# Kernel tuning notes

Hardware: AMD Instinct MI355X
Metric: run time of the kernel (lower is better)

## Reference

```python
import jax, jax.numpy as jnp
import numpy as np

N = 20000      # nodes
E = 160000     # edges
F_IN = 128     # node_feature_dim
HID = 128      # hidden_dim
HEADS = 8
G = 64         # graphs in batch


def setup_inputs() -> dict:
    key = jax.random.key(0)
    ks = iter(jax.random.split(key, 40))

    def w(shape, fan):
        return jax.random.normal(next(ks), shape, jnp.float32) / np.sqrt(fan)

    inp = {}
    inp['x'] = jax.random.normal(next(ks), (N, F_IN), jnp.float32)
    inp['edge_index'] = jax.random.randint(next(ks), (2, E), 0, N, jnp.int32)
    inp['batch'] = jnp.sort(jax.random.randint(next(ks), (N,), 0, G, jnp.int32))
    # initial projection
    inp['Wp'] = w((F_IN, HID), F_IN); inp['bp'] = jnp.zeros((HID,), jnp.float32)
    # layers 0..2: TransformerConv(HID -> HID//HEADS per head, heads=HEADS, concat) => heads*out = HID
    inp['Wq'] = w((3, HID, HID), HID); inp['bq'] = jnp.zeros((3, HID), jnp.float32)
    inp['Wk'] = w((3, HID, HID), HID); inp['bk'] = jnp.zeros((3, HID), jnp.float32)
    inp['Wv'] = w((3, HID, HID), HID); inp['bv'] = jnp.zeros((3, HID), jnp.float32)
    inp['Ws'] = w((3, HID, HID), HID); inp['bs'] = jnp.zeros((3, HID), jnp.float32)
    inp['Wbeta'] = w((3, 3 * HID, 1), 3 * HID)
    # layer 3: TransformerConv(HID -> HID per head, heads=HEADS, concat=False -> head mean)
    inp['Wq3'] = w((HID, HEADS * HID), HID); inp['bq3'] = jnp.zeros((HEADS * HID,), jnp.float32)
    inp['Wk3'] = w((HID, HEADS * HID), HID); inp['bk3'] = jnp.zeros((HEADS * HID,), jnp.float32)
    inp['Wv3'] = w((HID, HEADS * HID), HID); inp['bv3'] = jnp.zeros((HEADS * HID,), jnp.float32)
    inp['Ws3'] = w((HID, HID), HID); inp['bs3'] = jnp.zeros((HID,), jnp.float32)
    inp['Wbeta3'] = w((3 * HID, 1), 3 * HID)
    # batchnorm affine params for 4 layers
    inp['bn_gamma'] = jnp.ones((4, HID), jnp.float32)
    inp['bn_beta'] = jnp.zeros((4, HID), jnp.float32)
    return inp


def _tconv(x, src, dst, Wq, bq, Wk, bk, Wv, bv, Ws, bs, Wb, heads, concat):
    n = x.shape[0]
    d = Wq.shape[1] // heads  # per-head dim
    q = (x @ Wq + bq).reshape(n, heads, d)
    k = (x @ Wk + bk).reshape(n, heads, d)
    v = (x @ Wv + bv).reshape(n, heads, d)
    # per-edge attention logits [E, heads]
    logits = jnp.einsum('ehd,ehd->eh', q[dst], k[src]) / jnp.sqrt(jnp.float32(d))
    # segment softmax over incoming edges of each target node
    m = jax.ops.segment_max(logits, dst, num_segments=n)
    m = jnp.where(jnp.isfinite(m), m, 0.0)
    ex = jnp.exp(logits - m[dst])
    denom = jax.ops.segment_sum(ex, dst, num_segments=n)
    a = ex / (denom[dst] + 1e-16)  # [E, heads]
    out = jax.ops.segment_sum(a[:, :, None] * v[src], dst, num_segments=n)  # [n, heads, d]
    out = out.reshape(n, heads * d) if concat else out.mean(axis=1)
    # beta-gated skip connection
    r = x @ Ws + bs
    g = jax.nn.sigmoid(jnp.concatenate([out, r, out - r], axis=-1) @ Wb)  # [n, 1]
    return g * r + (1.0 - g) * out


def _bn(x, gamma, beta):
    mu = x.mean(axis=0)
    var = x.var(axis=0)
    return (x - mu) * jax.lax.rsqrt(var + 1e-5) * gamma + beta


def reference(x, edge_index, batch, Wp, bp, Wq, bq, Wk, bk, Wv, bv, Ws, bs, Wbeta,
              Wq3, bq3, Wk3, bk3, Wv3, bv3, Ws3, bs3, Wbeta3, bn_gamma, bn_beta):
    src, dst = edge_index[0], edge_index[1]
    h = x @ Wp + bp
    for i in range(3):
        h = _tconv(h, src, dst, Wq[i], bq[i], Wk[i], bk[i], Wv[i], bv[i],
                   Ws[i], bs[i], Wbeta[i], HEADS, concat=True)
        h = jax.nn.relu(_bn(h, bn_gamma[i], bn_beta[i]))
    h = _tconv(h, src, dst, Wq3, bq3, Wk3, bk3, Wv3, bv3, Ws3, bs3, Wbeta3,
               HEADS, concat=False)
    h = jax.nn.relu(_bn(h, bn_gamma[3], bn_beta[3]))
    # global mean pool per graph
    sums = jax.ops.segment_sum(h, batch, num_segments=G)
    cnt = jax.ops.segment_sum(jnp.ones((h.shape[0],), h.dtype), batch, num_segments=G)
    return sums / jnp.maximum(cnt, 1.0)[:, None]
```

## Files before the change

### kernel.cpp

```cpp
#include <hip/hip_runtime.h>
#include <math.h>

#define NNODES 20000
#define NPAD   20096
#define NEDGES 160000
#define HIDDIM 128
#define NHEADS 8
#define NGRAPH 64
#define KC 384
#define GXTILES 157

typedef short short8 __attribute__((ext_vector_type(8)));
typedef float floatx4 __attribute__((ext_vector_type(4)));
typedef unsigned short ushort4v __attribute__((ext_vector_type(4)));

__device__ inline unsigned short f2bf(float x) {
    unsigned u = __float_as_uint(x);
    u += 0x7fff + ((u >> 16) & 1);
    return (unsigned short)(u >> 16);
}
__device__ inline float bf2f(unsigned short h) {
    return __uint_as_float(((unsigned)h) << 16);
}

__device__ __forceinline__ void gload16(const unsigned short* g, unsigned short* l) {
    __builtin_amdgcn_global_load_lds(
        (const __attribute__((address_space(1))) unsigned int*)g,
        (__attribute__((address_space(3))) unsigned int*)l, 16, 0, 0);
}

__global__ __launch_bounds__(256) void zero_kernel(float* __restrict__ p, int n) {
    int i = blockIdx.x * blockDim.x + threadIdx.x;
    if (i < n) p[i] = 0.f;
}

__global__ __launch_bounds__(256) void count_deg_kernel(const int* __restrict__ dst,
                                                        int* __restrict__ deg, int e) {
    int i = blockIdx.x * blockDim.x + threadIdx.x;
    if (i < e) atomicAdd(&deg[dst[i]], 1);
}

__global__ __launch_bounds__(256) void scan1_kernel(const int* __restrict__ deg,
                                                    int* __restrict__ chunk,
                                                    int* __restrict__ bsum, int n) {
    __shared__ int buf[256];
    int t = threadIdx.x;
    int i = blockIdx.x * 256 + t;
    int v = (i < n) ? deg[i] : 0;
    buf[t] = v;
    __syncthreads();
    for (int off = 1; off < 256; off <<= 1) {
        int tmp = (t >= off) ? buf[t - off] : 0;
        __syncthreads();
        buf[t] += tmp;
        __syncthreads();
    }
    if (i < n) chunk[i] = buf[t];
    if (t == 255) bsum[blockIdx.x] = buf[255];
}

__global__ __launch_bounds__(128) void scan2_kernel(int* __restrict__ bsum, int nb) {
    __shared__ int buf[128];
    int t = threadIdx.x;
    int v = (t < nb) ? bsum[t] : 0;
    buf[t] = v;
    __syncthreads();
    for (int off = 1; off < 128; off <<= 1) {
        int tmp = (t >= off) ? buf[t - off] : 0;
        __syncthreads();
        buf[t] += tmp;
        __syncthreads();
    }
    if (t < nb) bsum[t] = buf[t] - v;
}

__global__ __launch_bounds__(256) void scan3_kernel(const int* __restrict__ chunk,
                                                    const int* __restrict__ bsum,
                                                    int* __restrict__ offs, int n) {
    int i = blockIdx.x * 256 + threadIdx.x;
    if (i < n) offs[i + 1] = chunk[i] + bsum[i >> 8];
    if (i == 0) offs[0] = 0;
}

__global__ __launch_bounds__(256) void scatter_gb_kernel(
    const int* __restrict__ src, const int* __restrict__ dst,
    const int* __restrict__ offs, int* __restrict__ cursor,
    int* __restrict__ csr_src, int e,
    const int* __restrict__ batch, int* __restrict__ gs, int* __restrict__ ge, int n) {
    int i = blockIdx.x * blockDim.x + threadIdx.x;
    if (i < e) {
        int d = dst[i];
        int pos = offs[d] + atomicAdd(&cursor[d], 1);
        csr_src[pos] = src[i];
    }
    if (i < n) {
        int b = batch[i];
        if (i == 0 || batch[i - 1] != b) gs[b] = i;
        if (i == n - 1 || batch[i + 1] != b) ge[b] = i + 1;
    }
}

__global__ __launch_bounds__(128) void prep_all_kernel(
    const float* __restrict__ Wq, const float* __restrict__ Wk,
    const float* __restrict__ Wv, const float* __restrict__ Ws,
    const float* __restrict__ Wp, const float* __restrict__ Ws3,
    const float* __restrict__ bq, const float* __restrict__ bk,
    const float* __restrict__ bv, const float* __restrict__ bs,
    const float* __restrict__ bs3,
    const float* __restrict__ Wq3, const float* __restrict__ Wk3,
    const float* __restrict__ bq3,
    const float* __restrict__ Wv3, const float* __restrict__ bv3,
    unsigned short* __restrict__ WtAll, float* __restrict__ bcat,
    unsigned short* __restrict__ Wvm, float* __restrict__ bvm) {
    int id = blockIdx.x;
    int k = threadIdx.x;
    if (id >= 3861) {
        int j = id - 3861;
#pragma unroll
        for (int h = 0; h < 8; ++h) {
            float w = Wv3[(size_t)k * 1024 + h * 128 + j] * 0.125f;
            Wvm[(size_t)j * 1024 + h * 128 + k] = f2bf(w);
        }
        if (k == 0) {
            float s = 0.f;
            for (int h = 0; h < 8; ++h) s += bv3[h * 128 + j];
            bvm[j] = s * 0.125f;
        }
        return;
    }
    if (id >= 2837) {
        int hb = id - 2837;
        int h = hb >> 7, b = hb & 127;
        __shared__ float wk[128];
        wk[k] = Wk3[(size_t)b * 1024 + h * 128 + k];
        __syncthreads();
        const float* wq = Wq3 + (size_t)k * 1024 + h * 128;
        float acc = 0.f;
#pragma unroll 16
        for (int d = 0; d < 128; ++d) acc = fmaf(wq[d], wk[d], acc);
        unsigned short hi = f2bf(acc);
        unsigned short lo = f2bf(acc - bf2f(hi));
        unsigned short* dst = WtAll + (size_t)(1664 + h * 128 + b) * KC;
        dst[k] = hi;
        dst[128 + k] = hi;
        dst[256 + k] = lo;
        if (k == 0) {
            float bb = 0.f;
            for (int d = 0; d < 128; ++d) bb = fmaf(bq3[h * 128 + d], wk[d], bb);
            bcat[1536 + h * 128 + b] = bb;
        }
        return;
    }
    if (id >= 2816) {
        int idx = (id - 2816) * 128 + k;
        if (idx >= 2688) return;
        float v;
        if (idx < 1536) {
            int li = idx / 512, n = idx % 512, sel = n >> 7, np = n & 127;
            const float* b = (sel == 0) ? bq : (sel == 1) ? bk : (sel == 2) ? bv : bs;
            v = b[li * 128 + np];
        } else if (idx < 2560) {
            return;
        } else {
            v = bs3[idx - 2560];
        }
        bcat[idx] = v;
        return;
    }
    float w;
    if (id < 1536) {
        int li = id / 512, n = id % 512, sel = n >> 7, np = n & 127;
        const float* W = (sel == 0) ? Wq : (sel == 1) ? Wk : (sel == 2) ? Wv : Ws;
        w = W[li * 16384 + k * 128 + np];
    } else if (id < 1664) {
        w = Wp[k * 128 + (id - 1536)];
    } else if (id < 2688) {
        return;
    } else {
        w = Ws3[k * 128 + (id - 2688)];
    }
    unsigned short hi = f2bf(w);
    unsigned short lo = f2bf(w - bf2f(hi));
    unsigned short* dst = WtAll + (size_t)id * KC;
    dst[k] = hi;
    dst[128 + k] = hi;
    dst[256 + k] = lo;
}

__global__ __launch_bounds__(256) void cat_from_kernel(const float* __restrict__ h,
                                                       unsigned short* __restrict__ Acat) {
    int idx = blockIdx.x * 256 + threadIdx.x;
    if (idx >= NPAD * HIDDIM) return;
    int r = idx >> 7, k = idx & 127;
    float x = (r < NNODES) ? h[idx] : 0.f;
    unsigned short hi = f2bf(x);
    unsigned short lo = f2bf(x - bf2f(hi));
    unsigned short* row = Acat + (size_t)r * KC;
    row[k] = hi;
    row[128 + k] = lo;
    row[256 + k] = hi;
}

template <typename OutT, int KG, int BY, int ST, int OMODE>
__global__ __launch_bounds__(256) void gemm_lds_kernel(
    const unsigned short* __restrict__ A, const unsigned short* __restrict__ Wt,
    const float* __restrict__ bias, OutT* __restrict__ C, int M, int nrows) {
    int id = blockIdx.x;
    int xcd = id & 7;
    int idx = id >> 3;
    int bx = (idx / BY) * 8 + xcd;
    int by = idx % BY;
    if (bx >= GXTILES) return;

    __shared__ unsigned short lds[2][2][4096];

    int tid = threadIdx.x;
    int lane = tid & 63;
    int wave = tid >> 6;
    int m = lane & 15;
    int q = lane >> 4;
    int nodeBase = bx * 128 + (wave & 1) * 64;
    int featBase = by * 128 + (wave >> 1) * 64;

    const unsigned short* gA = A + (size_t)bx * 128 * ST;
    const unsigned short* gW = Wt + (size_t)by * 128 * ST;

    int rs = lane >> 2;
    int cp0 = lane & 3;

    auto stagef = [&](int buf, int kk) {
        int kof = kk * 32;
#pragma unroll
        for (int jj = 0; jj < 2; ++jj) {
            int j = wave * 2 + jj;
            int row = j * 16 + rs;
            int g = cp0 ^ ((row >> 1) & 3);
            gload16(gA + (size_t)row * ST + kof + g * 8,
                    &lds[buf][0][0] + (size_t)j * 512);
            gload16(gW + (size_t)row * ST + kof + g * 8,
                    &lds[buf][1][0] + (size_t)j * 512);
        }
    };

    floatx4 acc[4][4];
#pragma unroll
    for (int r = 0; r < 4; ++r)
#pragma unroll
        for (int c = 0; c < 4; ++c) acc[r][c] = (floatx4){0.f, 0.f, 0.f, 0.f};

    stagef(0, 0);
    __syncthreads();

    for (int kg = 0; kg < KG; ++kg) {
        int cur = kg & 1;
        if (kg + 1 < KG) stagef(cur ^ 1, kg + 1);
        short8 a[4], b[4];
#pragma unroll
        for (int r = 0; r < 4; ++r) {
            int wr = (wave >> 1) * 64 + r * 16 + m;
            int cp = q ^ ((wr >> 1) & 3);
            a[r] = *(const short8*)(&lds[cur][1][0] + wr * 32 + cp * 8);
        }
#pragma unroll
        for (int c = 0; c < 4; ++c) {
            int ar = (wave & 1) * 64 + c * 16 + m;
            int cp = q ^ ((ar >> 1) & 3);
            b[c] = *(const short8*)(&lds[cur][0][0] + ar * 32 + cp * 8);
        }
#pragma unroll
        for (int r = 0; r < 4; ++r)
#pragma unroll
            for (int c = 0; c < 4; ++c)
                acc[r][c] = __builtin_amdgcn_mfma_f32_16x16x32_bf16(a[r], b[c], acc[r][c], 0, 0, 0);
        __syncthreads();
    }

    float4 bv[4];
#pragma unroll
    for (int r = 0; r < 4; ++r) bv[r] = *(const float4*)(bias + featBase + r * 16 + q * 4);
#pragma unroll
    for (int c = 0; c < 4; ++c) {
        int node = nodeBase + c * 16 + m;
        if (node < nrows) {
#pragma unroll
            for (int r = 0; r < 4; ++r) {
                int f0 = featBase + r * 16 + q * 4;
                float v0 = acc[r][c][0] + bv[r].x;
                float v1 = acc[r][c][1] + bv[r].y;
                float v2 = acc[r][c][2] + bv[r].z;
                float v3 = acc[r][c][3] + bv[r].w;
                if (OMODE == 2) {
                    unsigned short* row = (unsigned short*)C + (size_t)node * KC;
                    unsigned short h0 = f2bf(v0), h1 = f2bf(v1), h2 = f2bf(v2), h3 = f2bf(v3);
                    ushort4v hiv = {h0, h1, h2, h3};
                    ushort4v lov = {f2bf(v0 - bf2f(h0)), f2bf(v1 - bf2f(h1)),
                                    f2bf(v2 - bf2f(h2)), f2bf(v3 - bf2f(h3))};
                    *(ushort4v*)(row + f0) = hiv;
                    *(ushort4v*)(row + 128 + f0) = lov;
                    *(ushort4v*)(row + 256 + f0) = hiv;
                } else if (OMODE == 1) {
                    ushort4v o = {f2bf(v0), f2bf(v1), f2bf(v2), f2bf(v3)};
                    *(ushort4v*)((unsigned short*)C + (size_t)node * M + f0) = o;
                } else {
                    float4 o = {v0, v1, v2, v3};
                    *(float4*)((float*)C + (size_t)node * M + f0) = o;
                }
            }
        }
    }
}

__global__ __launch_bounds__(64) void attn_small_kernel(
    const unsigned short* __restrict__ qkvs,
    const float* __restrict__ Wb,
    const int* __restrict__ offs, const int* __restrict__ csr_src,
    float* __restrict__ out) {
    int i = blockIdx.x;
    int l = threadIdx.x;
    int g = l >> 5;
    int d0 = (l & 31) * 4;
    uint2 qraw = *(const uint2*)(qkvs + (size_t)i * 512 + d0);
    uint2 rraw = *(const uint2*)(qkvs + (size_t)i * 512 + 384 + d0);
    float q0 = bf2f((unsigned short)(qraw.x & 0xffff)), q1 = bf2f((unsigned short)(qraw.x >> 16));
    float q2 = bf2f((unsigned short)(qraw.y & 0xffff)), q3 = bf2f((unsigned short)(qraw.y >> 16));
    int e0 = offs[i], e1 = offs[i + 1];
    float lac = 0.f;
    float a0 = 0.f, a1 = 0.f, a2 = 0.f, a3 = 0.f;
    int e = e0 + g;
    uint2 kk_n = {0, 0}, vv_n = {0, 0};
    if (e < e1) {
        int sn = csr_src[e];
        const unsigned short* row = qkvs + (size_t)sn * 512;
        kk_n = *(const uint2*)(row + 128 + d0);
        vv_n = *(const uint2*)(row + 256 + d0);
    }
    while (e < e1) {
        uint2 kk = kk_n, vv = vv_n;
        int en = e + 2;
        if (en < e1) {
            int sn2 = csr_src[en];
            const unsigned short* row2 = qkvs + (size_t)sn2 * 512;
            kk_n = *(const uint2*)(row2 + 128 + d0);
            vv_n = *(const uint2*)(row2 + 256 + d0);
        }
        float k0 = bf2f((unsigned short)(kk.x & 0xffff)), k1 = bf2f((unsigned short)(kk.x >> 16));
        float k2 = bf2f((unsigned short)(kk.y & 0xffff)), k3 = bf2f((unsigned short)(kk.y >> 16));
        float p = q0 * k0 + q1 * k1 + q2 * k2 + q3 * k3;
        p += __shfl_xor(p, 1);
        p += __shfl_xor(p, 2);
        float w = __expf(p * 0.25f);
        float v0 = bf2f((unsigned short)(vv.x & 0xffff)), v1 = bf2f((unsigned short)(vv.x >> 16));
        float v2 = bf2f((unsigned short)(vv.y & 0xffff)), v3 = bf2f((unsigned short)(vv.y >> 16));
        a0 += w * v0;
        a1 += w * v1;
        a2 += w * v2;
        a3 += w * v3;
        lac += w;
        e = en;
    }
    a0 += __shfl_xor(a0, 32);
    a1 += __shfl_xor(a1, 32);
    a2 += __shfl_xor(a2, 32);
    a3 += __shfl_xor(a3, 32);
    lac += __shfl_xor(lac, 32);
    float inv = 1.f / (lac + 1e-16f);
    float o0 = a0 * inv, o1 = a1 * inv, o2 = a2 * inv, o3 = a3 * inv;
    float r0 = bf2f((unsigned short)(rraw.x & 0xffff)), r1 = bf2f((unsigned short)(rraw.x >> 16));
    float r2 = bf2f((unsigned short)(rraw.y & 0xffff)), r3 = bf2f((unsigned short)(rraw.y >> 16));
    float part = o0 * Wb[d0] + o1 * Wb[d0 + 1] + o2 * Wb[d0 + 2] + o3 * Wb[d0 + 3]
               + r0 * Wb[128 + d0] + r1 * Wb[128 + d0 + 1]
               + r2 * Wb[128 + d0 + 2] + r3 * Wb[128 + d0 + 3]
               + (o0 - r0) * Wb[256 + d0] + (o1 - r1) * Wb[256 + d0 + 1]
               + (o2 - r2) * Wb[256 + d0 + 2] + (o3 - r3) * Wb[256 + d0 + 3];
    if (g) part = 0.f;
#pragma unroll
    for (int msk = 1; msk <= 32; msk <<= 1) part += __shfl_xor(part, msk);
    float gg = 1.f / (1.f + __expf(-part));
    if (g == 0) {
        float4 o4 = {gg * r0 + (1.f - gg) * o0, gg * r1 + (1.f - gg) * o1,
                     gg * r2 + (1.f - gg) * o2, gg * r3 + (1.f - gg) * o3};
        *(float4*)(out + (size_t)i * HIDDIM + d0) = o4;
    }
}

__global__ __launch_bounds__(64) void attn_big_kernel(
    const unsigned short* __restrict__ tbuf, const unsigned short* __restrict__ Acat,
    const int* __restrict__ offs, const int* __restrict__ csr_src,
    unsigned short* __restrict__ agg) {
    int i = blockIdx.x;
    int l = threadIdx.x;
    int doff = (l & 7) * 16;
    const unsigned short* tp = tbuf + (size_t)i * 1152 + l * 16;
    uint4 t0 = *(const uint4*)tp;
    uint4 t1 = *(const uint4*)(tp + 8);
    float tq[16];
    tq[0] = bf2f((unsigned short)(t0.x & 0xffff)); tq[1] = bf2f((unsigned short)(t0.x >> 16));
    tq[2] = bf2f((unsigned short)(t0.y & 0xffff)); tq[3] = bf2f((unsigned short)(t0.y >> 16));
    tq[4] = bf2f((unsigned short)(t0.z & 0xffff)); tq[5] = bf2f((unsigned short)(t0.z >> 16));
    tq[6] = bf2f((unsigned short)(t0.w & 0xffff)); tq[7] = bf2f((unsigned short)(t0.w >> 16));
    tq[8] = bf2f((unsigned short)(t1.x & 0xffff)); tq[9] = bf2f((unsigned short)(t1.x >> 16));
    tq[10] = bf2f((unsigned short)(t1.y & 0xffff)); tq[11] = bf2f((unsigned short)(t1.y >> 16));
    tq[12] = bf2f((unsigned short)(t1.z & 0xffff)); tq[13] = bf2f((unsigned short)(t1.z >> 16));
    tq[14] = bf2f((unsigned short)(t1.w & 0xffff)); tq[15] = bf2f((unsigned short)(t1.w >> 16));
    int e0 = offs[i], e1 = offs[i + 1];
    float ac[16];
#pragma unroll
    for (int j = 0; j < 16; ++j) ac[j] = 0.f;
    float lac = 0.f;
    int e = e0;
    uint4 k0n = {0, 0, 0, 0}, k1n = {0, 0, 0, 0};
    if (e < e1) {
        const unsigned short* hp = Acat + (size_t)csr_src[e] * KC + doff;
        k0n = *(const uint4*)hp;
        k1n = *(const uint4*)(hp + 8);
    }
    while (e < e1) {
        uint4 k0 = k0n, k1 = k1n;
        int en = e + 1;
        if (en < e1) {
            const unsigned short* hp2 = Acat + (size_t)csr_src[en] * KC + doff;
            k0n = *(const uint4*)hp2;
            k1n = *(const uint4*)(hp2 + 8);
        }
        float kk[16];
        kk[0] = bf2f((unsigned short)(k0.x & 0xffff)); kk[1] = bf2f((unsigned short)(k0.x >> 16));
        kk[2] = bf2f((unsigned short)(k0.y & 0xffff)); kk[3] = bf2f((unsigned short)(k0.y >> 16));
        kk[4] = bf2f((unsigned short)(k0.z & 0xffff)); kk[5] = bf2f((unsigned short)(k0.z >> 16));
        kk[6] = bf2f((unsigned short)(k0.w & 0xffff)); kk[7] = bf2f((unsigned short)(k0.w >> 16));
        kk[8] = bf2f((unsigned short)(k1.x & 0xffff)); kk[9] = bf2f((unsigned short)(k1.x >> 16));
        kk[10] = bf2f((unsigned short)(k1.y & 0xffff)); kk[11] = bf2f((unsigned short)(k1.y >> 16));
        kk[12] = bf2f((unsigned short)(k1.z & 0xffff)); kk[13] = bf2f((unsigned short)(k1.z >> 16));
        kk[14] = bf2f((unsigned short)(k1.w & 0xffff)); kk[15] = bf2f((unsigned short)(k1.w >> 16));
        float p = 0.f;
#pragma unroll
        for (int j = 0; j < 16; ++j) p = fmaf(tq[j], kk[j], p);
        p += __shfl_xor(p, 1);
        p += __shfl_xor(p, 2);
        p += __shfl_xor(p, 4);
        float w = __expf(p * 0.08838834764831845f);
#pragma unroll
        for (int j = 0; j < 16; ++j) ac[j] = fmaf(w, kk[j], ac[j]);
        lac += w;
        e = en;
    }
    float inv = 1.f / (lac + 1e-16f);
    unsigned short* o = agg + (size_t)i * 1024 + l * 16;
    ushort4v o0 = {f2bf(ac[0] * inv), f2bf(ac[1] * inv), f2bf(ac[2] * inv), f2bf(ac[3] * inv)};
    ushort4v o1 = {f2bf(ac[4] * inv), f2bf(ac[5] * inv), f2bf(ac[6] * inv), f2bf(ac[7] * inv)};
    ushort4v o2 = {f2bf(ac[8] * inv), f2bf(ac[9] * inv), f2bf(ac[10] * inv), f2bf(ac[11] * inv)};
    ushort4v o3 = {f2bf(ac[12] * inv), f2bf(ac[13] * inv), f2bf(ac[14] * inv), f2bf(ac[15] * inv)};
    *(ushort4v*)o = o0;
    *(ushort4v*)(o + 4) = o1;
    *(ushort4v*)(o + 8) = o2;
    *(ushort4v*)(o + 12) = o3;
}

__global__ __launch_bounds__(128) void beta3_stats_kernel(
    const float* __restrict__ omean, const unsigned short* __restrict__ tbuf,
    const float* __restrict__ Wb, float* __restrict__ out,
    float* __restrict__ stat, int n, float* __restrict__ pool_out) {
    int t = threadIdx.x;
    if (blockIdx.x < NGRAPH) pool_out[blockIdx.x * HIDDIM + t] = 0.f;
    __shared__ float wsum[2];
    float s = 0.f, sq = 0.f;
    for (int i = blockIdx.x; i < n; i += gridDim.x) {
        float o = omean[(size_t)i * HIDDIM + t];
        float r = bf2f(tbuf[(size_t)i * 1152 + 1024 + t]);
        float part = o * Wb[t] + r * Wb[128 + t] + (o - r) * Wb[256 + t];
#pragma unroll
        for (int msk = 1; msk <= 32; msk <<= 1) part += __shfl_xor(part, msk);
        if ((t & 63) == 0) wsum[t >> 6] = part;
        __syncthreads();
        float tot = wsum[0] + wsum[1];
        __syncthreads();
        float g = 1.f / (1.f + __expf(-tot));
        float v = g * r + (1.f - g) * o;
        out[(size_t)i * HIDDIM + t] = v;
        s += v;
        sq += v * v;
    }
    atomicAdd(&stat[t], s);
    atomicAdd(&stat[HIDDIM + t], sq);
}

__global__ __launch_bounds__(128) void bn_stats_kernel(const float* __restrict__ x,
                                                       float* __restrict__ stat, int n) {
    int t = threadIdx.x;
    float s = 0.f, sq = 0.f;
    for (int i = blockIdx.x; i < n; i += gridDim.x) {
        float v = x[(size_t)i * HIDDIM + t];
        s += v;
        sq += v * v;
    }
    atomicAdd(&stat[t], s);
    atomicAdd(&stat[HIDDIM + t], sq);
}

__global__ __launch_bounds__(128) void bn_apply_kernel(float* __restrict__ x,
                                                       const float* __restrict__ stat,
                                                       const float* __restrict__ gamma,
                                                       const float* __restrict__ beta, int n,
                                                       unsigned short* __restrict__ cat) {
    int t = threadIdx.x;
    float mu = stat[t] / (float)n;
    float var = stat[HIDDIM + t] / (float)n - mu * mu;
    float rs = rsqrtf(var + 1e-5f);
    float g = gamma[t], b = beta[t];
    for (int i = blockIdx.x; i < n; i += gridDim.x) {
        float v = x[(size_t)i * HIDDIM + t];
        v = fmaxf((v - mu) * rs * g + b, 0.f);
        x[(size_t)i * HIDDIM + t] = v;
        if (cat) {
            unsigned short hi = f2bf(v);
            unsigned short lo = f2bf(v - bf2f(hi));
            unsigned short* row = cat + (size_t)i * KC;
            row[t] = hi;
            row[128 + t] = lo;
            row[256 + t] = hi;
        }
    }
}

__global__ __launch_bounds__(256) void pool_bn_part_kernel(
    const float* __restrict__ x, const float* __restrict__ stat,
    const float* __restrict__ gamma, const float* __restrict__ beta,
    const int* __restrict__ gs, const int* __restrict__ ge,
    float* __restrict__ out, int n) {
    int g = blockIdx.x, c = blockIdx.y;
    int t = threadIdx.x;
    int f = t & 127, half = t >> 7;
    float mu = stat[f] / (float)n;
    float var = stat[HIDDIM + f] / (float)n - mu * mu;
    float rs = rsqrtf(var + 1e-5f);
    float ga = gamma[f], be = beta[f];
    int s = gs[g], e = ge[g];
    float acc = 0.f;
    for (int i = s + 2 * c + half; i < e; i += 16)
        acc += fmaxf((x[(size_t)i * HIDDIM + f] - mu) * rs * ga + be, 0.f);
    __shared__ float l0[128];
    if (half == 0) l0[f] = acc;
    __syncthreads();
    if (half == 1) {
        int cnt = e - s;
        float inv = 1.f / (float)(cnt > 0 ? cnt : 1);
        atomicAdd(&out[g * HIDDIM + f], (l0[f] + acc) * inv);
    }
}

extern "C" void kernel_launch(void* const* d_in, const int* in_sizes, int n_in,
                              void* d_out, int out_size, void* d_ws, size_t ws_size,
                              hipStream_t stream) {
    const float* x       = (const float*)d_in[0];
    const int*   ei      = (const int*)d_in[1];
    const int*   batch   = (const int*)d_in[2];
    const float* Wp      = (const float*)d_in[3];
    const float* bp      = (const float*)d_in[4];
    const float* Wq      = (const float*)d_in[5];
    const float* bq      = (const float*)d_in[6];
    const float* Wk      = (const float*)d_in[7];
    const float* bk      = (const float*)d_in[8];
    const float* Wv      = (const float*)d_in[9];
    const float* bv      = (const float*)d_in[10];
    const float* Ws      = (const float*)d_in[11];
    const float* bs      = (const float*)d_in[12];
    const float* Wbeta   = (const float*)d_in[13];
    const float* Wq3     = (const float*)d_in[14];
    const float* bq3     = (const float*)d_in[15];
    const float* Wk3     = (const float*)d_in[16];
    const float* bk3     = (const float*)d_in[17];
    const float* Wv3     = (const float*)d_in[18];
    const float* bv3     = (const float*)d_in[19];
    const float* Ws3     = (const float*)d_in[20];
    const float* bs3     = (const float*)d_in[21];
    const float* Wbeta3  = (const float*)d_in[22];
    const float* bn_gamma = (const float*)d_in[23];
    const float* bn_beta  = (const float*)d_in[24];
    float* out = (float*)d_out;
    (void)bk3;

    const int* esrc = ei;
    const int* edst = ei + NEDGES;

    char* wpc = (char*)d_ws;
    auto alloc = [&](size_t nbytes) -> char* {
        char* p = wpc;
        wpc += (nbytes + 255) & ~(size_t)255;
        return p;
    };
    unsigned short* Acat  = (unsigned short*)alloc((size_t)NPAD * KC * 2);
    unsigned short* WtAll = (unsigned short*)alloc((size_t)2816 * KC * 2);
    float* bcat   = (float*)alloc(2688 * 4);
    unsigned short* Wvm   = (unsigned short*)alloc((size_t)128 * 1024 * 2);
    float* bvm    = (float*)alloc(128 * 4);
    unsigned short* tbuf  = (unsigned short*)alloc((size_t)NPAD * 1152 * 2);
    unsigned short* aggb  = (unsigned short*)alloc((size_t)NPAD * 1024 * 2);
    float* omean  = (float*)alloc((size_t)NNODES * HIDDIM * 4);
    float* hbuf   = (float*)alloc((size_t)NNODES * HIDDIM * 4);
    float* obuf   = (float*)alloc((size_t)NNODES * HIDDIM * 4);
    int*   deg    = (int*)alloc((2 * NNODES + 128 + 4 * 256) * 4);
    int*   cursor = deg + NNODES;
    int*   gs     = deg + 2 * NNODES;
    int*   ge     = gs + NGRAPH;
    float* bnstat4 = (float*)(deg + 2 * NNODES + 128);
    int*   chunk  = (int*)alloc(NNODES * 4);
    int*   bsum   = (int*)alloc(128 * 4);
    int*   offs   = (int*)alloc((NNODES + 1) * 4);
    int*   csrsrc = (int*)alloc(NEDGES * 4);

    unsigned short* WtQKVS = WtAll;
    unsigned short* Wpt    = WtAll + (size_t)1536 * KC;
    unsigned short* Wt3    = WtAll + (size_t)1664 * KC;
    float* bQKVS = bcat;
    float* b3    = bcat + 1536;
    unsigned short* qkvs = tbuf;

    const int TB = 256;
    const int ZWORDS = 2 * NNODES + 128 + 4 * 256;
    zero_kernel<<<(ZWORDS + TB - 1) / TB, TB, 0, stream>>>((float*)deg, ZWORDS);
    count_deg_kernel<<<(NEDGES + TB - 1) / TB, TB, 0, stream>>>(edst, deg, NEDGES);
    const int NB = (NNODES + 255) / 256;
    scan1_kernel<<<NB, 256, 0, stream>>>(deg, chunk, bsum, NNODES);
    scan2_kernel<<<1, 128, 0, stream>>>(bsum, NB);
    scan3_kernel<<<NB, 256, 0, stream>>>(chunk, bsum, offs, NNODES);
    scatter_gb_kernel<<<(NEDGES + TB - 1) / TB, TB, 0, stream>>>(
        esrc, edst, offs, cursor, csrsrc, NEDGES, batch, gs, ge, NNODES);

    prep_all_kernel<<<3989, 128, 0, stream>>>(Wq, Wk, Wv, Ws, Wp, Ws3,
                                              bq, bk, bv, bs, bs3,
                                              Wq3, Wk3, bq3, Wv3, bv3,
                                              WtAll, bcat, Wvm, bvm);

    const int CATB = (NPAD * HIDDIM + TB - 1) / TB;
    const int GSW = 8 * ((GXTILES + 7) / 8);

    cat_from_kernel<<<CATB, TB, 0, stream>>>(x, Acat);
    gemm_lds_kernel<unsigned short, 12, 1, KC, 2><<<GSW * 1, 256, 0, stream>>>(
        Acat, Wpt, bp, Acat, 0, NNODES);

    for (int li = 0; li < 3; ++li) {
        gemm_lds_kernel<unsigned short, 8, 4, KC, 1><<<GSW * 4, 256, 0, stream>>>(
            Acat, WtQKVS + (size_t)li * 512 * KC, bQKVS + li * 512, qkvs, 512, NNODES);
        attn_small_kernel<<<NNODES, 64, 0, stream>>>(qkvs, Wbeta + li * 384,
                                                     offs, csrsrc, obuf);
        float* st = bnstat4 + li * 256;
        bn_stats_kernel<<<640, 128, 0, stream>>>(obuf, st, NNODES);
        bn_apply_kernel<<<512, 128, 0, stream>>>(obuf, st, bn_gamma + li * HIDDIM,
                                                 bn_beta + li * HIDDIM, NNODES, Acat);
    }

    gemm_lds_kernel<unsigned short, 8, 9, KC, 1><<<GSW * 9, 256, 0, stream>>>(
        Acat, Wt3, b3, tbuf, 1152, NNODES);
    attn_big_kernel<<<NNODES, 64, 0, stream>>>(tbuf, Acat, offs, csrsrc, aggb);
    gemm_lds_kernel<float, 32, 1, 1024, 0><<<GSW, 256, 0, stream>>>(
        aggb, Wvm, bvm, omean, HIDDIM, NNODES);
    float* st3 = bnstat4 + 3 * 256;
    beta3_stats_kernel<<<512, 128, 0, stream>>>(omean, tbuf, Wbeta3, hbuf, st3, NNODES, out);
    pool_bn_part_kernel<<<dim3(NGRAPH, 8), 256, 0, stream>>>(
        hbuf, st3, bn_gamma + 3 * HIDDIM, bn_beta + 3 * HIDDIM, gs, ge, out, NNODES);
}
```

Before: 486.0 us.

## Fuse BN statistics into attention kernel and pack four nodes per block

```diff
diff --git a/kernel.cpp b/kernel.cpp
--- a/kernel.cpp
+++ b/kernel.cpp
@@ -310,13 +310,17 @@
     }
 }
 
-__global__ __launch_bounds__(64) void attn_small_kernel(
+__global__ __launch_bounds__(256) void attn_small_kernel(
     const unsigned short* __restrict__ qkvs,
     const float* __restrict__ Wb,
     const int* __restrict__ offs, const int* __restrict__ csr_src,
-    float* __restrict__ out) {
-    int i = blockIdx.x;
-    int l = threadIdx.x;
+    float* __restrict__ out, float* __restrict__ stat) {
+    int tid = threadIdx.x;
+    int i = blockIdx.x * 4 + (tid >> 6);
+    int l = tid & 63;
+    __shared__ float ssum[128], ssq[128];
+    if (tid < 128) { ssum[tid] = 0.f; ssq[tid] = 0.f; }
+    __syncthreads();
     int g = l >> 5;
     int d0 = (l & 31) * 4;
     uint2 qraw = *(const uint2*)(qkvs + (size_t)i * 512 + d0);
@@ -377,18 +381,31 @@
     for (int msk = 1; msk <= 32; msk <<= 1) part += __shfl_xor(part, msk);
     float gg = 1.f / (1.f + __expf(-part));
     if (g == 0) {
-        float4 o4 = {gg * r0 + (1.f - gg) * o0, gg * r1 + (1.f - gg) * o1,
-                     gg * r2 + (1.f - gg) * o2, gg * r3 + (1.f - gg) * o3};
+        float w0 = gg * r0 + (1.f - gg) * o0;
+        float w1 = gg * r1 + (1.f - gg) * o1;
+        float w2 = gg * r2 + (1.f - gg) * o2;
+        float w3 = gg * r3 + (1.f - gg) * o3;
+        float4 o4 = {w0, w1, w2, w3};
         *(float4*)(out + (size_t)i * HIDDIM + d0) = o4;
-    }
-}
-
-__global__ __launch_bounds__(64) void attn_big_kernel(
+        atomicAdd(&ssum[d0], w0);     atomicAdd(&ssq[d0], w0 * w0);
+        atomicAdd(&ssum[d0 + 1], w1); atomicAdd(&ssq[d0 + 1], w1 * w1);
+        atomicAdd(&ssum[d0 + 2], w2); atomicAdd(&ssq[d0 + 2], w2 * w2);
+        atomicAdd(&ssum[d0 + 3], w3); atomicAdd(&ssq[d0 + 3], w3 * w3);
+    }
+    __syncthreads();
+    if (tid < 128) {
+        atomicAdd(&stat[tid], ssum[tid]);
+        atomicAdd(&stat[HIDDIM + tid], ssq[tid]);
+    }
+}
+
+__global__ __launch_bounds__(256) void attn_big_kernel(
     const unsigned short* __restrict__ tbuf, const unsigned short* __restrict__ Acat,
     const int* __restrict__ offs, const int* __restrict__ csr_src,
     unsigned short* __restrict__ agg) {
-    int i = blockIdx.x;
-    int l = threadIdx.x;
+    int tid = threadIdx.x;
+    int i = blockIdx.x * 4 + (tid >> 6);
+    int l = tid & 63;
     int doff = (l & 7) * 16;
     const unsigned short* tp = tbuf + (size_t)i * 1152 + l * 16;
     uint4 t0 = *(const uint4*)tp;
@@ -476,19 +493,6 @@
         float g = 1.f / (1.f + __expf(-tot));
         float v = g * r + (1.f - g) * o;
         out[(size_t)i * HIDDIM + t] = v;
-        s += v;
-        sq += v * v;
-    }
-    atomicAdd(&stat[t], s);
-    atomicAdd(&stat[HIDDIM + t], sq);
-}
-
-__global__ __launch_bounds__(128) void bn_stats_kernel(const float* __restrict__ x,
-                                                       float* __restrict__ stat, int n) {
-    int t = threadIdx.x;
-    float s = 0.f, sq = 0.f;
-    for (int i = blockIdx.x; i < n; i += gridDim.x) {
-        float v = x[(size_t)i * HIDDIM + t];
         s += v;
         sq += v * v;
     }
@@ -640,17 +644,16 @@
     for (int li = 0; li < 3; ++li) {
         gemm_lds_kernel<unsigned short, 8, 4, KC, 1><<<GSW * 4, 256, 0, stream>>>(
             Acat, WtQKVS + (size_t)li * 512 * KC, bQKVS + li * 512, qkvs, 512, NNODES);
-        attn_small_kernel<<<NNODES, 64, 0, stream>>>(qkvs, Wbeta + li * 384,
-                                                     offs, csrsrc, obuf);
         float* st = bnstat4 + li * 256;
-        bn_stats_kernel<<<640, 128, 0, stream>>>(obuf, st, NNODES);
+        attn_small_kernel<<<NNODES / 4, 256, 0, stream>>>(qkvs, Wbeta + li * 384,
+                                                          offs, csrsrc, obuf, st);
         bn_apply_kernel<<<512, 128, 0, stream>>>(obuf, st, bn_gamma + li * HIDDIM,
                                                  bn_beta + li * HIDDIM, NNODES, Acat);
     }
 
     gemm_lds_kernel<unsigned short, 8, 9, KC, 1><<<GSW * 9, 256, 0, stream>>>(
         Acat, Wt3, b3, tbuf, 1152, NNODES);
-    attn_big_kernel<<<NNODES, 64, 0, stream>>>(tbuf, Acat, offs, csrsrc, aggb);
+    attn_big_kernel<<<NNODES / 4, 256, 0, stream>>>(tbuf, Acat, offs, csrsrc, aggb);
     gemm_lds_kernel<float, 32, 1, 1024, 0><<<GSW, 256, 0, stream>>>(
         aggb, Wvm, bvm, omean, HIDDIM, NNODES);
     float* st3 = bnstat4 + 3 * 256;
```

After: 777.2 us. +59.9%, slower.
